# Kernel tuning notes

Measured on AMD Instinct MI355X. Metric: run time of the kernel, lower is better.

The kernel has to match this reference:

```python
import jax, jax.numpy as jnp
import numpy as np

NUM_FREQS = 256
FRAME_SIZE = 5
LOOKAHEAD = 0

B, T, F_TOTAL = 8, 4096, 481


def setup_inputs() -> dict:
    key = jax.random.key(0)
    k1, k2 = jax.random.split(key)
    spec = jax.random.normal(k1, (B, 2, T, F_TOTAL), dtype=jnp.float32)
    coefs = jax.random.normal(k2, (B, 2 * FRAME_SIZE, T, NUM_FREQS), dtype=jnp.float32)
    return {"spec": spec, "coefs": coefs}


def reference(spec, coefs):
    # spec:  [B, 2, T, F_total]  (real/imag channels)
    # coefs: [B, 2*frame_size, T, num_freqs]
    Bc, _, Tc, Fq = coefs.shape
    df = spec[..., :NUM_FREQS]  # [B, 2, T, Fq]
    # causal pad along time: (frame_size-1-lookahead) before, lookahead after
    padded = jnp.pad(df, ((0, 0), (0, 0), (FRAME_SIZE - 1 - LOOKAHEAD, LOOKAHEAD), (0, 0)))
    # unfold over time -> [B, 2, T, Fq, frame_size]
    frames = jnp.stack([padded[:, :, k:k + Tc, :] for k in range(FRAME_SIZE)], axis=-1)
    # coefs -> [B, 2, T, Fq, frame_size]
    c = coefs.reshape(Bc, 2, FRAME_SIZE, Tc, Fq).transpose(0, 1, 3, 4, 2)
    pr, pi = frames[:, 0], frames[:, 1]
    cr, ci = c[:, 0], c[:, 1]
    real = jnp.sum(pr * cr - pi * ci, axis=-1)  # [B, T, Fq]
    imag = jnp.sum(pi * cr + pr * ci, axis=-1)
    spec_f = jnp.stack([real, imag], axis=1)    # [B, 2, T, Fq]
    return jnp.concatenate([spec_f, spec[..., NUM_FREQS:]], axis=-1)
```

## Files before the change

kernel.cpp:

```cpp
#include <hip/hip_runtime.h>


static constexpr int kB  = 8;
static constexpr int kT  = 4096;
static constexpr int kFT = 481;
static constexpr int kNF = 256;
static constexpr int kFS = 5;
static constexpr int kTT = 4;
static constexpr int kWin = kTT + kFS - 1;
static constexpr int kTailF = kFT - kNF;
static constexpr unsigned kTailElems = (unsigned)kB * 2u * kT * kTailF;

typedef float v4f __attribute__((ext_vector_type(4)));

__global__ __launch_bounds__(256) void df_fused(const float* __restrict__ spec,
                                                const float* __restrict__ coefs,
                                                float* __restrict__ out) {
    const int idx = blockIdx.x * 256 + threadIdx.x;
    const int f4 = idx & 63;
    const int b  = (idx >> 6) & 7;
    const int tg = idx >> 9;
    const int t0 = tg * kTT;
    const int f  = f4 << 2;

    const float* sr = spec + (size_t)(b * 2    ) * kT * kFT + f;
    const float* si = spec + (size_t)(b * 2 + 1) * kT * kFT + f;

    float prw[kWin][4];
    float piw[kWin][4];
#pragma unroll
    for (int r = 0; r < kWin; ++r) {
        const int tk = t0 - (kFS - 1) + r;
        if (tk >= 0) {
            const float* pr = sr + (size_t)tk * kFT;
            const float* pi = si + (size_t)tk * kFT;
#pragma unroll
            for (int j = 0; j < 4; ++j) { prw[r][j] = pr[j]; piw[r][j] = pi[j]; }
        } else {
#pragma unroll
            for (int j = 0; j < 4; ++j) { prw[r][j] = 0.f; piw[r][j] = 0.f; }
        }
    }

#pragma unroll
    for (int tt = 0; tt < kTT; ++tt) {
        const int t = t0 + tt;
        float accR[4] = {0.f, 0.f, 0.f, 0.f};
        float accI[4] = {0.f, 0.f, 0.f, 0.f};
#pragma unroll
        for (int k = 0; k < kFS; ++k) {
            const v4f cr = __builtin_nontemporal_load(
                (const v4f*)(coefs + ((size_t)(b * 10 + k    ) * kT + t) * kNF + f));
            const v4f ci = __builtin_nontemporal_load(
                (const v4f*)(coefs + ((size_t)(b * 10 + 5 + k) * kT + t) * kNF + f));
            const int r = tt + k;
#pragma unroll
            for (int j = 0; j < 4; ++j) {
                accR[j] = fmaf(prw[r][j], cr[j], fmaf(-piw[r][j], ci[j], accR[j]));
                accI[j] = fmaf(piw[r][j], cr[j], fmaf( prw[r][j], ci[j], accI[j]));
            }
        }
        float* oR = out + ((size_t)(b * 2    ) * kT + t) * kFT + f;
        float* oI = out + ((size_t)(b * 2 + 1) * kT + t) * kFT + f;
#pragma unroll
        for (int j = 0; j < 4; ++j) {
            __builtin_nontemporal_store(accR[j], oR + j);
            __builtin_nontemporal_store(accI[j], oI + j);
        }
    }

    const unsigned gsz = gridDim.x * 256u;
    for (unsigned i = (unsigned)idx; i < kTailElems; i += gsz) {
        const unsigned row = i / (unsigned)kTailF;
        const unsigned col = i - row * (unsigned)kTailF;
        const size_t off = (size_t)row * kFT + kNF + col;
        __builtin_nontemporal_store(__builtin_nontemporal_load(spec + off), out + off);
    }
}

extern "C" void kernel_launch(void* const* d_in, const int* in_sizes, int n_in,
                              void* d_out, int out_size, void* d_ws, size_t ws_size,
                              hipStream_t stream) {
    const float* spec  = (const float*)d_in[0];
    const float* coefs = (const float*)d_in[1];
    float* out = (float*)d_out;

    df_fused<<<(kB * (kT / kTT) * (kNF / 4)) / 256, 256, 0, stream>>>(spec, coefs, out);
}
```

Baseline: 567.2 us.

## Stride per-thread frequencies by 64 and swizzle block order across XCDs

```diff
diff --git a/kernel.cpp b/kernel.cpp
--- a/kernel.cpp
+++ b/kernel.cpp
@@ -10,21 +10,20 @@
 static constexpr int kWin = kTT + kFS - 1;
 static constexpr int kTailF = kFT - kNF;
 static constexpr unsigned kTailElems = (unsigned)kB * 2u * kT * kTailF;
-
-typedef float v4f __attribute__((ext_vector_type(4)));
+static constexpr int kGrid = (kB * (kT / kTT) * (kNF / 4)) / 256;
 
 __global__ __launch_bounds__(256) void df_fused(const float* __restrict__ spec,
                                                 const float* __restrict__ coefs,
                                                 float* __restrict__ out) {
-    const int idx = blockIdx.x * 256 + threadIdx.x;
+    const int lbid = (blockIdx.x & 7) * (kGrid / 8) + (blockIdx.x >> 3);
+    const int idx  = lbid * 256 + (int)threadIdx.x;
     const int f4 = idx & 63;
     const int b  = (idx >> 6) & 7;
     const int tg = idx >> 9;
     const int t0 = tg * kTT;
-    const int f  = f4 << 2;
 
-    const float* sr = spec + (size_t)(b * 2    ) * kT * kFT + f;
-    const float* si = spec + (size_t)(b * 2 + 1) * kT * kFT + f;
+    const float* sr = spec + (size_t)(b * 2) * kT * kFT + f4;
+    const float* si = sr + (size_t)kT * kFT;
 
     float prw[kWin][4];
     float piw[kWin][4];
@@ -35,7 +34,7 @@
             const float* pr = sr + (size_t)tk * kFT;
             const float* pi = si + (size_t)tk * kFT;
 #pragma unroll
-            for (int j = 0; j < 4; ++j) { prw[r][j] = pr[j]; piw[r][j] = pi[j]; }
+            for (int j = 0; j < 4; ++j) { prw[r][j] = pr[64 * j]; piw[r][j] = pi[64 * j]; }
         } else {
 #pragma unroll
             for (int j = 0; j < 4; ++j) { prw[r][j] = 0.f; piw[r][j] = 0.f; }
@@ -49,28 +48,28 @@
         float accI[4] = {0.f, 0.f, 0.f, 0.f};
 #pragma unroll
         for (int k = 0; k < kFS; ++k) {
-            const v4f cr = __builtin_nontemporal_load(
-                (const v4f*)(coefs + ((size_t)(b * 10 + k    ) * kT + t) * kNF + f));
-            const v4f ci = __builtin_nontemporal_load(
-                (const v4f*)(coefs + ((size_t)(b * 10 + 5 + k) * kT + t) * kNF + f));
+            const float* cb = coefs + ((size_t)(b * 10 + k) * kT + t) * kNF + f4;
             const int r = tt + k;
 #pragma unroll
             for (int j = 0; j < 4; ++j) {
-                accR[j] = fmaf(prw[r][j], cr[j], fmaf(-piw[r][j], ci[j], accR[j]));
-                accI[j] = fmaf(piw[r][j], cr[j], fmaf( prw[r][j], ci[j], accI[j]));
+                const float cr = __builtin_nontemporal_load(cb + 64 * j);
+                const float ci = __builtin_nontemporal_load(cb + (size_t)5 * kT * kNF + 64 * j);
+                accR[j] = fmaf(prw[r][j], cr, fmaf(-piw[r][j], ci, accR[j]));
+                accI[j] = fmaf(piw[r][j], cr, fmaf( prw[r][j], ci, accI[j]));
             }
         }
-        float* oR = out + ((size_t)(b * 2    ) * kT + t) * kFT + f;
-        float* oI = out + ((size_t)(b * 2 + 1) * kT + t) * kFT + f;
+        float* oR = out + ((size_t)(b * 2) * kT + t) * kFT + f4;
+        float* oI = oR + (size_t)kT * kFT;
 #pragma unroll
         for (int j = 0; j < 4; ++j) {
-            __builtin_nontemporal_store(accR[j], oR + j);
-            __builtin_nontemporal_store(accI[j], oI + j);
+            __builtin_nontemporal_store(accR[j], oR + 64 * j);
+            __builtin_nontemporal_store(accI[j], oI + 64 * j);
         }
     }
 
-    const unsigned gsz = gridDim.x * 256u;
-    for (unsigned i = (unsigned)idx; i < kTailElems; i += gsz) {
+    const int ridx = (int)blockIdx.x * 256 + (int)threadIdx.x;
+    const unsigned gsz = (unsigned)kGrid * 256u;
+    for (unsigned i = (unsigned)ridx; i < kTailElems; i += gsz) {
         const unsigned row = i / (unsigned)kTailF;
         const unsigned col = i - row * (unsigned)kTailF;
         const size_t off = (size_t)row * kFT + kNF + col;
@@ -85,5 +84,5 @@
     const float* coefs = (const float*)d_in[1];
     float* out = (float*)d_out;
 
-    df_fused<<<(kB * (kT / kTT) * (kNF / 4)) / 256, 256, 0, stream>>>(spec, coefs, out);
+    df_fused<<<kGrid, 256, 0, stream>>>(spec, coefs, out);
 }
```

Measured after the change: 565.5 us. No clear change (-0.3%).
